# Kernel optimization log

Measured on AMD Instinct MI355X. Metric: run time of the kernel, lower is better.

## Reference

```python
import jax, jax.numpy as jnp
import numpy as np


def _phase_idx(phase):
    t = 4.0 * phase
    i1 = jnp.mod(jnp.floor(t).astype(jnp.int32), 4)
    i0 = jnp.mod(i1 - 1, 4)
    i2 = jnp.mod(i1 + 1, 4)
    i3 = jnp.mod(i1 + 2, 4)
    w = jnp.mod(t, 1.0)  # fmod(t,1) for t>=0
    return w, i0, i1, i2, i3


def _cubic(a0, a1, a2, a3, w):
    # Catmull-Rom spline blend; a* have shape (B, ...), w broadcastable
    return (a1
            + w * (0.5 * a2 - 0.5 * a0)
            + w * w * (a0 - 2.5 * a1 + 2.0 * a2 - 0.5 * a3)
            + w * w * w * (1.5 * a1 - 1.5 * a2 + 0.5 * a3 - 0.5 * a0))


def setup_inputs() -> dict:
    key = jax.random.key(0)
    ks = jax.random.split(key, 8)
    B = 4096
    dims = [128, 256, 256, 128]

    def kaiming(k, shape):
        fan_in = shape[1]
        bound = np.sqrt(6.0 / fan_in)
        return jax.random.uniform(k, shape, jnp.float32, -bound, bound)

    inp = {
        "x": jax.random.normal(ks[0], (B, dims[0]), jnp.float32),
        "phase": jax.random.uniform(ks[1], (B,), jnp.float32),
    }
    for i in range(3):
        inp[f"w{i}"] = kaiming(ks[2 + i], (4, dims[i], dims[i + 1]))
        inp[f"b{i}"] = jnp.zeros((4, 1, dims[i + 1]), jnp.float32)
    return inp


def reference(x, phase, w0, b0, w1, b1, w2, b2):
    ws = [w0, w1, w2]
    bs = [b0, b1, b2]
    w, i0, i1, i2, i3 = _phase_idx(phase)
    w3 = w[:, None, None]  # (B,1,1) for weights and biases
    n = len(ws)
    for li in range(n):
        pw, pb = ws[li], bs[li]
        # per-sample interpolated weight (B, in, out) and bias (B, 1, out)
        weight = _cubic(pw[i0], pw[i1], pw[i2], pw[i3], w3)
        bias = _cubic(pb[i0], pb[i1], pb[i2], pb[i3], w3)
        x = jnp.einsum("bi,bio->bo", x, weight) + bias[:, 0, :]
        if li < n - 1:  # activation_at_last=False
            x = jax.nn.elu(x)
    return x
```

## Files before the change

kernel.cpp:

```cpp
#include <hip/hip_runtime.h>
#include <hip/hip_bf16.h>
#include <math.h>


typedef __attribute__((ext_vector_type(8))) short bf16x8;
typedef __attribute__((ext_vector_type(4))) float f32x4;

#define LDS_A0 0
#define LDS_A1 4096
#define LDS_A2 12288
#define LDS_B  20480
#define LDS_TOT (20480 + 131072)

#define VMW4()  asm volatile("s_waitcnt vmcnt(4)" ::: "memory")
#define VMW0()  asm volatile("s_waitcnt vmcnt(0)" ::: "memory")

static __device__ __forceinline__ void bar_keep_vmcnt() {
  asm volatile("s_waitcnt lgkmcnt(0)" ::: "memory");
  __builtin_amdgcn_s_barrier();
  asm volatile("" ::: "memory");
}

typedef const __attribute__((address_space(1))) unsigned char* gp1_t;
typedef __attribute__((address_space(3))) unsigned char* lp3_t;
static __device__ __forceinline__ void gl_lds16(const void* g, void* l) {
  __builtin_amdgcn_global_load_lds((gp1_t)g, (lp3_t)l, 16, 0, 0);
}

#define STAGE(sb, KIN, ci, slot) do {                                  \
    const unsigned short* _s = (sb) + (ci) * 32;                       \
    char* _d = myB + (slot) * 4096;                                    \
    gl_lds16(_s,             _d);                                      \
    gl_lds16(_s + (KIN),     _d + 1024);                               \
    gl_lds16(_s + 2 * (KIN), _d + 2048);                               \
    gl_lds16(_s + 3 * (KIN), _d + 3072);                               \
  } while (0)

static __device__ __forceinline__ unsigned short f2bf(float f) {
  union { float f; unsigned int u; } v; v.f = f;
  unsigned int r = v.u + 0x7fffu + ((v.u >> 16) & 1u);
  return (unsigned short)(r >> 16);
}

static __device__ __forceinline__ void catmull(float ph, float c[4]) {
  float t = 4.0f * ph;
  float ft = floorf(t);
  int i1 = ((int)ft) & 3;
  float w = t - ft;
  float w2 = w * w, w3 = w2 * w;
  float r0 = -0.5f * w + w2 - 0.5f * w3;
  float r1 = 1.0f - 2.5f * w2 + 1.5f * w3;
  float r2 = 0.5f * w + 2.0f * w2 - 1.5f * w3;
  float r3 = -0.5f * w2 + 0.5f * w3;
  c[(i1 + 3) & 3] = r0;
  c[i1]           = r1;
  c[(i1 + 1) & 3] = r2;
  c[(i1 + 2) & 3] = r3;
}

__global__ void k_wt_all(const float* __restrict__ w0, const float* __restrict__ w1,
                         const float* __restrict__ w2, unsigned short* __restrict__ t0,
                         unsigned short* __restrict__ t1, unsigned short* __restrict__ t2) {
  __shared__ float tile[32][33];
  int bid = blockIdx.x;
  const float* W; unsigned short* T; int R, C, idx;
  if (bid < 128)      { W = w0; T = t0; R = 512;  C = 256; idx = bid; }
  else if (bid < 384) { W = w1; T = t1; R = 1024; C = 256; idx = bid - 128; }
  else                { W = w2; T = t2; R = 1024; C = 128; idx = bid - 384; }
  int ntc = C >> 5;
  int tr = (idx / ntc) << 5;
  int tc = (idx % ntc) << 5;
  int tx = threadIdx.x, ty = threadIdx.y;
#pragma unroll
  for (int j = ty; j < 32; j += 8)
    tile[j][tx] = W[(size_t)(tr + j) * C + (tc + tx)];
  __syncthreads();
#pragma unroll
  for (int j = ty; j < 32; j += 8)
    T[(size_t)(tc + j) * R + (tr + tx)] = f2bf(tile[tx][j]);
}

static __device__ __forceinline__ void epi_mid(f32x4 a0, f32x4 a1, f32x4 a2, f32x4 a3,
                                               const float bm[4], const float cbr[4][4],
                                               int colg, int quad, char* outBuf) {
  const int g = colg >> 3;
  const int j2 = (colg & 7) * 2;
#pragma unroll
  for (int r = 0; r < 4; ++r) {
    const int m = quad * 4 + r;
    float y = cbr[r][0] * a0[r] + cbr[r][1] * a1[r] +
              cbr[r][2] * a2[r] + cbr[r][3] * a3[r] + bm[r];
    float a = y > 0.0f ? y : (__expf(y) - 1.0f);
    *(unsigned short*)(outBuf + m * 512 + (((g ^ (m & 15)) << 4) + j2)) = f2bf(a);
  }
}

#define MFMA4()                                                            \
  acc0 = __builtin_amdgcn_mfma_f32_16x16x32_bf16(av, bv0, acc0, 0, 0, 0);  \
  acc1 = __builtin_amdgcn_mfma_f32_16x16x32_bf16(av, bv1, acc1, 0, 0, 0);  \
  acc2 = __builtin_amdgcn_mfma_f32_16x16x32_bf16(av, bv2, acc2, 0, 0, 0);  \
  acc3 = __builtin_amdgcn_mfma_f32_16x16x32_bf16(av, bv3, acc3, 0, 0, 0)

#define LOADB()                                                \
  bf16x8 bv0 = *(const bf16x8*)(bs + bOff);                    \
  bf16x8 bv1 = *(const bf16x8*)(bs + 1024 + bOff);             \
  bf16x8 bv2 = *(const bf16x8*)(bs + 2048 + bOff);             \
  bf16x8 bv3 = *(const bf16x8*)(bs + 3072 + bOff)

__global__ __launch_bounds__(1024, 4) void k_fused(
    const float* __restrict__ x, const float* __restrict__ phase,
    const unsigned short* __restrict__ Wt0, const float* __restrict__ b0,
    const unsigned short* __restrict__ Wt1, const float* __restrict__ b1,
    const unsigned short* __restrict__ Wt2, const float* __restrict__ b2,
    float* __restrict__ out) {
  __shared__ __align__(1024) char smem[LDS_TOT];

  const int tid = threadIdx.x;
  const int lane = tid & 63;
  const int wid = tid >> 6;
  const int col = lane & 15;
  const int quad = lane >> 4;
  const int m0 = blockIdx.x * 16;
  const int colg = wid * 16 + col;
  const int cg = wid & 7, kh = wid >> 3;
  const int colg2 = cg * 16 + col;
  const int hi16 = (col & 12) << 4;
  const int lb = (quad ^ (col & 3)) << 4;
  const int bOff = col * 64 + quad * 16;

  char* myB = smem + LDS_B + wid * 8192;

  const int colL = lane >> 2, qs = lane & 3;
  const unsigned short* sb0 = Wt0 + (size_t)(wid * 16 + colL) * 512 + qs * 8;
  const unsigned short* sb1 = Wt1 + (size_t)(wid * 16 + colL) * 1024 + qs * 8;
  const unsigned short* sb2 = Wt2 + (size_t)(cg * 16 + colL) * 1024 + kh * 128 + qs * 8;

  float bva[4], bvb[4], bvc[4];
#pragma unroll
  for (int k = 0; k < 4; ++k) {
    bva[k] = b0[k * 256 + colg];
    bvb[k] = b1[k * 256 + colg];
    bvc[k] = b2[k * 128 + colg2];
  }
  float ph[4];
#pragma unroll
  for (int r = 0; r < 4; ++r) ph[r] = phase[m0 + quad * 4 + r];

  float4 xv = {0.f, 0.f, 0.f, 0.f};
  if (tid < 512)
    xv = *(const float4*)(x + (size_t)(m0 + (tid >> 5)) * 128 + (tid & 31) * 4);

  STAGE(sb0, 128, 0, 0);

  float cbr[4][4];
#pragma unroll
  for (int r = 0; r < 4; ++r) catmull(ph[r], cbr[r]);
  float bm0[4], bm1[4], bm2[4];
#pragma unroll
  for (int r = 0; r < 4; ++r) {
    bm0[r] = cbr[r][0] * bva[0] + cbr[r][1] * bva[1] + cbr[r][2] * bva[2] + cbr[r][3] * bva[3];
    bm1[r] = cbr[r][0] * bvb[0] + cbr[r][1] * bvb[1] + cbr[r][2] * bvb[2] + cbr[r][3] * bvb[3];
    bm2[r] = cbr[r][0] * bvc[0] + cbr[r][1] * bvc[1] + cbr[r][2] * bvc[2] + cbr[r][3] * bvc[3];
  }

  if (tid < 512) {
    const int row = tid >> 5, seg = tid & 31;
    const int g = seg >> 1, h = seg & 1;
    short4 hv;
    hv.x = (short)f2bf(xv.x); hv.y = (short)f2bf(xv.y);
    hv.z = (short)f2bf(xv.z); hv.w = (short)f2bf(xv.w);
    *(short4*)(smem + LDS_A0 + row * 256 + ((g ^ (row & 15)) << 4) + h * 8) = hv;
  }
  bar_keep_vmcnt();

  f32x4 acc0, acc1, acc2, acc3;

  {
    acc0 = acc1 = acc2 = acc3 = (f32x4){0.f, 0.f, 0.f, 0.f};
    const char* aL = smem + LDS_A0 + col * 256 + lb;
#pragma unroll
    for (int i = 0; i < 4; ++i) {
      if (i < 3) STAGE(sb0, 128, i + 1, (i + 1) & 1);
      else       STAGE(sb1, 256, 0, 0);
      VMW4();
      const char* bs = myB + (i & 1) * 4096;
      bf16x8 av = *(const bf16x8*)(aL + ((i << 6) ^ hi16));
      LOADB();
      MFMA4();
    }
    epi_mid(acc0, acc1, acc2, acc3, bm0, cbr, colg, quad, smem + LDS_A1);
  }
  bar_keep_vmcnt();

  {
    acc0 = acc1 = acc2 = acc3 = (f32x4){0.f, 0.f, 0.f, 0.f};
    const char* aL = smem + LDS_A1 + col * 512 + lb;
#pragma unroll
    for (int i = 0; i < 8; ++i) {
      if (i < 7) STAGE(sb1, 256, i + 1, (i + 1) & 1);
      else       STAGE(sb2, 256, 0, 0);
      VMW4();
      const char* bs = myB + (i & 1) * 4096;
      bf16x8 av = *(const bf16x8*)(aL + ((i << 6) ^ hi16));
      LOADB();
      MFMA4();
    }
    epi_mid(acc0, acc1, acc2, acc3, bm1, cbr, colg, quad, smem + LDS_A2);
  }
  bar_keep_vmcnt();

  {
    acc0 = acc1 = acc2 = acc3 = (f32x4){0.f, 0.f, 0.f, 0.f};
    const char* aL = smem + LDS_A2 + col * 512 + kh * 256 + lb;
#pragma unroll
    for (int i = 0; i < 4; ++i) {
      if (i < 3) { STAGE(sb2, 256, i + 1, (i + 1) & 1); VMW4(); }
      else       { VMW0(); }
      const char* bs = myB + (i & 1) * 4096;
      bf16x8 av = *(const bf16x8*)(aL + ((i << 6) ^ hi16));
      LOADB();
      MFMA4();
    }

    float part[4];
#pragma unroll
    for (int r = 0; r < 4; ++r)
      part[r] = cbr[r][0] * acc0[r] + cbr[r][1] * acc1[r] +
                cbr[r][2] * acc2[r] + cbr[r][3] * acc3[r];

    bar_keep_vmcnt();
    float* red = (float*)(smem + LDS_B);
    if (kh) {
#pragma unroll
      for (int r = 0; r < 4; ++r)
        red[cg * 272 + (quad * 4 + r) * 17 + col] = part[r];
    }
    bar_keep_vmcnt();
    if (!kh) {
#pragma unroll
      for (int r = 0; r < 4; ++r) {
        const int m = quad * 4 + r;
        float y = part[r] + red[cg * 272 + m * 17 + col] + bm2[r];
        out[(size_t)(m0 + m) * 128 + colg2] = y;
      }
    }
  }
}

extern "C" void kernel_launch(void* const* d_in, const int* in_sizes, int n_in,
                              void* d_out, int out_size, void* d_ws, size_t ws_size,
                              hipStream_t stream) {
  const float* x     = (const float*)d_in[0];
  const float* phase = (const float*)d_in[1];
  const float* w0    = (const float*)d_in[2];
  const float* b0    = (const float*)d_in[3];
  const float* w1    = (const float*)d_in[4];
  const float* b1    = (const float*)d_in[5];
  const float* w2    = (const float*)d_in[6];
  const float* b2    = (const float*)d_in[7];
  float* out = (float*)d_out;

  char* ws = (char*)d_ws;
  unsigned short* Wt0 = (unsigned short*)ws;
  unsigned short* Wt1 = (unsigned short*)(ws + 262144);
  unsigned short* Wt2 = (unsigned short*)(ws + 262144 + 524288);

  k_wt_all<<<512, dim3(32, 8), 0, stream>>>(w0, w1, w2, Wt0, Wt1, Wt2);
  k_fused<<<256, 1024, 0, stream>>>(x, phase, Wt0, b0, Wt1, b1, Wt2, b2, out);
}
```

Before: 90.77 us.

## Stagger per-block weight chunk order and issue prefetch after LDS reads

Each block now rotates which wave handles which column group and starts each layer's K loop at a block-dependent chunk offset. The goal is to spread concurrent global reads across different weight addresses and channels. The staging pipeline also now prefetches two chunks ahead, issuing each new load only after the current LDS reads complete (lgkmcnt(0)), so buffers can be reused safely while keeping more loads in flight. This adds index arithmetic, and the extra lgkmcnt waits could stall MFMA issue.

Measured after the change: 93.75 us. 1.03x slower.

```diff
diff --git a/kernel.cpp b/kernel.cpp
--- a/kernel.cpp
+++ b/kernel.cpp
@@ -14,6 +14,7 @@
 
 #define VMW4()  asm volatile("s_waitcnt vmcnt(4)" ::: "memory")
 #define VMW0()  asm volatile("s_waitcnt vmcnt(0)" ::: "memory")
+#define LGKM0() asm volatile("s_waitcnt lgkmcnt(0)" ::: "memory")
 
 static __device__ __forceinline__ void bar_keep_vmcnt() {
   asm volatile("s_waitcnt lgkmcnt(0)" ::: "memory");
@@ -121,8 +122,15 @@
   const int col = lane & 15;
   const int quad = lane >> 4;
   const int m0 = blockIdx.x * 16;
-  const int colg = wid * 16 + col;
-  const int cg = wid & 7, kh = wid >> 3;
+
+  const int p = (int)(blockIdx.x >> 3);
+  const int wg = (wid + p) & 15;
+  const int cr0 = p & 3;
+  const int cr1 = (p + (p >> 2)) & 7;
+  const int cr2 = (p >> 1) & 3;
+
+  const int colg = wg * 16 + col;
+  const int cg = wg & 7, kh = wg >> 3;
   const int colg2 = cg * 16 + col;
   const int hi16 = (col & 12) << 4;
   const int lb = (quad ^ (col & 3)) << 4;
@@ -131,8 +139,8 @@
   char* myB = smem + LDS_B + wid * 8192;
 
   const int colL = lane >> 2, qs = lane & 3;
-  const unsigned short* sb0 = Wt0 + (size_t)(wid * 16 + colL) * 512 + qs * 8;
-  const unsigned short* sb1 = Wt1 + (size_t)(wid * 16 + colL) * 1024 + qs * 8;
+  const unsigned short* sb0 = Wt0 + (size_t)(wg * 16 + colL) * 512 + qs * 8;
+  const unsigned short* sb1 = Wt1 + (size_t)(wg * 16 + colL) * 1024 + qs * 8;
   const unsigned short* sb2 = Wt2 + (size_t)(cg * 16 + colL) * 1024 + kh * 128 + qs * 8;
 
   float bva[4], bvb[4], bvc[4];
@@ -150,7 +158,8 @@
   if (tid < 512)
     xv = *(const float4*)(x + (size_t)(m0 + (tid >> 5)) * 128 + (tid & 31) * 4);
 
-  STAGE(sb0, 128, 0, 0);
+  STAGE(sb0, 128, cr0, 0);
+  STAGE(sb0, 128, (1 + cr0) & 3, 1);
 
   float cbr[4][4];
 #pragma unroll
@@ -180,12 +189,16 @@
     const char* aL = smem + LDS_A0 + col * 256 + lb;
 #pragma unroll
     for (int i = 0; i < 4; ++i) {
-      if (i < 3) STAGE(sb0, 128, i + 1, (i + 1) & 1);
-      else       STAGE(sb1, 256, 0, 0);
       VMW4();
       const char* bs = myB + (i & 1) * 4096;
-      bf16x8 av = *(const bf16x8*)(aL + ((i << 6) ^ hi16));
+      const int ci = (i + cr0) & 3;
+      bf16x8 av = *(const bf16x8*)(aL + ((ci << 6) ^ hi16));
       LOADB();
+      LGKM0();
+      if (i == 0)      STAGE(sb0, 128, (2 + cr0) & 3, 0);
+      else if (i == 1) STAGE(sb0, 128, (3 + cr0) & 3, 1);
+      else if (i == 2) STAGE(sb1, 256, cr1, 0);
+      else             STAGE(sb1, 256, (1 + cr1) & 7, 1);
       MFMA4();
     }
     epi_mid(acc0, acc1, acc2, acc3, bm0, cbr, colg, quad, smem + LDS_A1);
@@ -197,12 +210,15 @@
     const char* aL = smem + LDS_A1 + col * 512 + lb;
 #pragma unroll
     for (int i = 0; i < 8; ++i) {
-      if (i < 7) STAGE(sb1, 256, i + 1, (i + 1) & 1);
-      else       STAGE(sb2, 256, 0, 0);
       VMW4();
       const char* bs = myB + (i & 1) * 4096;
-      bf16x8 av = *(const bf16x8*)(aL + ((i << 6) ^ hi16));
+      const int ci = (i + cr1) & 7;
+      bf16x8 av = *(const bf16x8*)(aL + ((ci << 6) ^ hi16));
       LOADB();
+      LGKM0();
+      if (i < 6)       STAGE(sb1, 256, (i + 2 + cr1) & 7, i & 1);
+      else if (i == 6) STAGE(sb2, 256, cr2, 0);
+      else             STAGE(sb2, 256, (1 + cr2) & 3, 1);
       MFMA4();
     }
     epi_mid(acc0, acc1, acc2, acc3, bm1, cbr, colg, quad, smem + LDS_A2);
@@ -214,11 +230,16 @@
     const char* aL = smem + LDS_A2 + col * 512 + kh * 256 + lb;
 #pragma unroll
     for (int i = 0; i < 4; ++i) {
-      if (i < 3) { STAGE(sb2, 256, i + 1, (i + 1) & 1); VMW4(); }
-      else       { VMW0(); }
+      if (i < 3) { VMW4(); } else { VMW0(); }
       const char* bs = myB + (i & 1) * 4096;
-      bf16x8 av = *(const bf16x8*)(aL + ((i << 6) ^ hi16));
+      const int ci = (i + cr2) & 3;
+      bf16x8 av = *(const bf16x8*)(aL + ((ci << 6) ^ hi16));
       LOADB();
+      if (i < 2) {
+        LGKM0();
+        if (i == 0) STAGE(sb2, 256, (2 + cr2) & 3, 0);
+        else        STAGE(sb2, 256, (3 + cr2) & 3, 1);
+      }
       MFMA4();
     }
 
```

## Prefetch weight fragments into registers instead of staging through LDS

Applied to the files above, without the earlier changes.

The fused kernel stops using global_load_lds staging buffers and explicit vmcnt waits. It now loads each wave's B-operand fragments directly into a three-deep register ring (pre[3][4]) that is prefetched ahead across layer boundaries. This shrinks LDS use from about 150KB to about 29KB. Bias is folded by initialising the accumulators with the per-phase bias, which is valid because the Catmull-Rom coefficients sum to one, so the separate bias blend is removed. The transpose kernel is repacked to four 32x32 tiles per 1024-thread block. Risks are higher register pressure and compiler-inserted waits on the direct global loads.

After: 101.3 us. 11.6% more time.

```diff
diff --git a/kernel.cpp b/kernel.cpp
--- a/kernel.cpp
+++ b/kernel.cpp
@@ -6,35 +6,17 @@
 typedef __attribute__((ext_vector_type(8))) short bf16x8;
 typedef __attribute__((ext_vector_type(4))) float f32x4;
 
-#define LDS_A0 0
-#define LDS_A1 4096
-#define LDS_A2 12288
-#define LDS_B  20480
-#define LDS_TOT (20480 + 131072)
-
-#define VMW4()  asm volatile("s_waitcnt vmcnt(4)" ::: "memory")
-#define VMW0()  asm volatile("s_waitcnt vmcnt(0)" ::: "memory")
-
-static __device__ __forceinline__ void bar_keep_vmcnt() {
+#define LDS_A0  0
+#define LDS_A1  4096
+#define LDS_A2  12288
+#define LDS_RED 20480
+#define LDS_TOT (20480 + 8704)
+
+static __device__ __forceinline__ void bar_lgkm() {
   asm volatile("s_waitcnt lgkmcnt(0)" ::: "memory");
   __builtin_amdgcn_s_barrier();
   asm volatile("" ::: "memory");
 }
-
-typedef const __attribute__((address_space(1))) unsigned char* gp1_t;
-typedef __attribute__((address_space(3))) unsigned char* lp3_t;
-static __device__ __forceinline__ void gl_lds16(const void* g, void* l) {
-  __builtin_amdgcn_global_load_lds((gp1_t)g, (lp3_t)l, 16, 0, 0);
-}
-
-#define STAGE(sb, KIN, ci, slot) do {                                  \
-    const unsigned short* _s = (sb) + (ci) * 32;                       \
-    char* _d = myB + (slot) * 4096;                                    \
-    gl_lds16(_s,             _d);                                      \
-    gl_lds16(_s + (KIN),     _d + 1024);                               \
-    gl_lds16(_s + 2 * (KIN), _d + 2048);                               \
-    gl_lds16(_s + 3 * (KIN), _d + 3072);                               \
-  } while (0)
 
 static __device__ __forceinline__ unsigned short f2bf(float f) {
   union { float f; unsigned int u; } v; v.f = f;
@@ -58,30 +40,49 @@
   c[(i1 + 2) & 3] = r3;
 }
 
-__global__ void k_wt_all(const float* __restrict__ w0, const float* __restrict__ w1,
-                         const float* __restrict__ w2, unsigned short* __restrict__ t0,
-                         unsigned short* __restrict__ t1, unsigned short* __restrict__ t2) {
-  __shared__ float tile[32][33];
-  int bid = blockIdx.x;
+__global__ __launch_bounds__(1024) void k_wt_all(
+    const float* __restrict__ w0, const float* __restrict__ w1,
+    const float* __restrict__ w2, unsigned short* __restrict__ t0,
+    unsigned short* __restrict__ t1, unsigned short* __restrict__ t2) {
+  __shared__ float tile[4][32][33];
+  const int team = threadIdx.y >> 3;
+  const int tyy = threadIdx.y & 7;
+  const int tx = threadIdx.x;
+  const int bid = blockIdx.x * 4 + team;
   const float* W; unsigned short* T; int R, C, idx;
   if (bid < 128)      { W = w0; T = t0; R = 512;  C = 256; idx = bid; }
   else if (bid < 384) { W = w1; T = t1; R = 1024; C = 256; idx = bid - 128; }
   else                { W = w2; T = t2; R = 1024; C = 128; idx = bid - 384; }
-  int ntc = C >> 5;
-  int tr = (idx / ntc) << 5;
-  int tc = (idx % ntc) << 5;
-  int tx = threadIdx.x, ty = threadIdx.y;
-#pragma unroll
-  for (int j = ty; j < 32; j += 8)
-    tile[j][tx] = W[(size_t)(tr + j) * C + (tc + tx)];
+  const int ntc = C >> 5;
+  const int tr = (idx / ntc) << 5;
+  const int tc = (idx % ntc) << 5;
+#pragma unroll
+  for (int j = tyy; j < 32; j += 8)
+    tile[team][j][tx] = W[(size_t)(tr + j) * C + (tc + tx)];
   __syncthreads();
 #pragma unroll
-  for (int j = ty; j < 32; j += 8)
-    T[(size_t)(tc + j) * R + (tr + tx)] = f2bf(tile[tx][j]);
-}
-
-static __device__ __forceinline__ void epi_mid(f32x4 a0, f32x4 a1, f32x4 a2, f32x4 a3,
-                                               const float bm[4], const float cbr[4][4],
+  for (int j = tyy; j < 32; j += 8)
+    T[(size_t)(tc + j) * R + (tr + tx)] = f2bf(tile[team][tx][j]);
+}
+
+#define LOADCH(sb, KA, ci, sl)                                       \
+  pre[sl][0] = *(const bf16x8*)((sb) + 0 * (KA) + (ci) * 32);        \
+  pre[sl][1] = *(const bf16x8*)((sb) + 1 * (KA) + (ci) * 32);        \
+  pre[sl][2] = *(const bf16x8*)((sb) + 2 * (KA) + (ci) * 32);        \
+  pre[sl][3] = *(const bf16x8*)((sb) + 3 * (KA) + (ci) * 32)
+
+#define MFMA4()                                                            \
+  acc0 = __builtin_amdgcn_mfma_f32_16x16x32_bf16(av, b0v, acc0, 0, 0, 0);  \
+  acc1 = __builtin_amdgcn_mfma_f32_16x16x32_bf16(av, b1v, acc1, 0, 0, 0);  \
+  acc2 = __builtin_amdgcn_mfma_f32_16x16x32_bf16(av, b2v, acc2, 0, 0, 0);  \
+  acc3 = __builtin_amdgcn_mfma_f32_16x16x32_bf16(av, b3v, acc3, 0, 0, 0)
+
+#define TAKE(sl)                                                     \
+  bf16x8 b0v = pre[sl][0], b1v = pre[sl][1],                         \
+         b2v = pre[sl][2], b3v = pre[sl][3]
+
+static __device__ __forceinline__ void epi_mid(f32x4 a0, f32x4 a1, f32x4 a2,
+                                               f32x4 a3, const float cbr[4][4],
                                                int colg, int quad, char* outBuf) {
   const int g = colg >> 3;
   const int j2 = (colg & 7) * 2;
@@ -89,23 +90,11 @@
   for (int r = 0; r < 4; ++r) {
     const int m = quad * 4 + r;
     float y = cbr[r][0] * a0[r] + cbr[r][1] * a1[r] +
-              cbr[r][2] * a2[r] + cbr[r][3] * a3[r] + bm[r];
+              cbr[r][2] * a2[r] + cbr[r][3] * a3[r];
     float a = y > 0.0f ? y : (__expf(y) - 1.0f);
     *(unsigned short*)(outBuf + m * 512 + (((g ^ (m & 15)) << 4) + j2)) = f2bf(a);
   }
 }
-
-#define MFMA4()                                                            \
-  acc0 = __builtin_amdgcn_mfma_f32_16x16x32_bf16(av, bv0, acc0, 0, 0, 0);  \
-  acc1 = __builtin_amdgcn_mfma_f32_16x16x32_bf16(av, bv1, acc1, 0, 0, 0);  \
-  acc2 = __builtin_amdgcn_mfma_f32_16x16x32_bf16(av, bv2, acc2, 0, 0, 0);  \
-  acc3 = __builtin_amdgcn_mfma_f32_16x16x32_bf16(av, bv3, acc3, 0, 0, 0)
-
-#define LOADB()                                                \
-  bf16x8 bv0 = *(const bf16x8*)(bs + bOff);                    \
-  bf16x8 bv1 = *(const bf16x8*)(bs + 1024 + bOff);             \
-  bf16x8 bv2 = *(const bf16x8*)(bs + 2048 + bOff);             \
-  bf16x8 bv3 = *(const bf16x8*)(bs + 3072 + bOff)
 
 __global__ __launch_bounds__(1024, 4) void k_fused(
     const float* __restrict__ x, const float* __restrict__ phase,
@@ -126,14 +115,14 @@
   const int colg2 = cg * 16 + col;
   const int hi16 = (col & 12) << 4;
   const int lb = (quad ^ (col & 3)) << 4;
-  const int bOff = col * 64 + quad * 16;
-
-  char* myB = smem + LDS_B + wid * 8192;
-
-  const int colL = lane >> 2, qs = lane & 3;
-  const unsigned short* sb0 = Wt0 + (size_t)(wid * 16 + colL) * 512 + qs * 8;
-  const unsigned short* sb1 = Wt1 + (size_t)(wid * 16 + colL) * 1024 + qs * 8;
-  const unsigned short* sb2 = Wt2 + (size_t)(cg * 16 + colL) * 1024 + kh * 128 + qs * 8;
+
+  const unsigned short* sb0 = Wt0 + (size_t)colg * 512 + quad * 8;
+  const unsigned short* sb1 = Wt1 + (size_t)colg * 1024 + quad * 8;
+  const unsigned short* sb2 = Wt2 + (size_t)colg2 * 1024 + kh * 128 + quad * 8;
+
+  float4 xv = {0.f, 0.f, 0.f, 0.f};
+  if (tid < 512)
+    xv = *(const float4*)(x + (size_t)(m0 + (tid >> 5)) * 128 + (tid & 31) * 4);
 
   float bva[4], bvb[4], bvc[4];
 #pragma unroll
@@ -146,22 +135,14 @@
 #pragma unroll
   for (int r = 0; r < 4; ++r) ph[r] = phase[m0 + quad * 4 + r];
 
-  float4 xv = {0.f, 0.f, 0.f, 0.f};
-  if (tid < 512)
-    xv = *(const float4*)(x + (size_t)(m0 + (tid >> 5)) * 128 + (tid & 31) * 4);
-
-  STAGE(sb0, 128, 0, 0);
+  bf16x8 pre[3][4];
+  LOADCH(sb0, 128, 0, 0);
+  LOADCH(sb0, 128, 1, 1);
+  LOADCH(sb0, 128, 2, 2);
 
   float cbr[4][4];
 #pragma unroll
   for (int r = 0; r < 4; ++r) catmull(ph[r], cbr[r]);
-  float bm0[4], bm1[4], bm2[4];
-#pragma unroll
-  for (int r = 0; r < 4; ++r) {
-    bm0[r] = cbr[r][0] * bva[0] + cbr[r][1] * bva[1] + cbr[r][2] * bva[2] + cbr[r][3] * bva[3];
-    bm1[r] = cbr[r][0] * bvb[0] + cbr[r][1] * bvb[1] + cbr[r][2] * bvb[2] + cbr[r][3] * bvb[3];
-    bm2[r] = cbr[r][0] * bvc[0] + cbr[r][1] * bvc[1] + cbr[r][2] * bvc[2] + cbr[r][3] * bvc[3];
-  }
 
   if (tid < 512) {
     const int row = tid >> 5, seg = tid & 31;
@@ -171,54 +152,65 @@
     hv.z = (short)f2bf(xv.z); hv.w = (short)f2bf(xv.w);
     *(short4*)(smem + LDS_A0 + row * 256 + ((g ^ (row & 15)) << 4) + h * 8) = hv;
   }
-  bar_keep_vmcnt();
+  bar_lgkm();
 
   f32x4 acc0, acc1, acc2, acc3;
 
   {
-    acc0 = acc1 = acc2 = acc3 = (f32x4){0.f, 0.f, 0.f, 0.f};
+    acc0 = (f32x4){bva[0], bva[0], bva[0], bva[0]};
+    acc1 = (f32x4){bva[1], bva[1], bva[1], bva[1]};
+    acc2 = (f32x4){bva[2], bva[2], bva[2], bva[2]};
+    acc3 = (f32x4){bva[3], bva[3], bva[3], bva[3]};
     const char* aL = smem + LDS_A0 + col * 256 + lb;
 #pragma unroll
     for (int i = 0; i < 4; ++i) {
-      if (i < 3) STAGE(sb0, 128, i + 1, (i + 1) & 1);
-      else       STAGE(sb1, 256, 0, 0);
-      VMW4();
-      const char* bs = myB + (i & 1) * 4096;
+      const int sl = i % 3;
+      TAKE(sl);
+      if (i == 0)      { LOADCH(sb0, 128, 3, 0); }
+      else if (i == 1) { LOADCH(sb1, 256, 0, 1); }
+      else if (i == 2) { LOADCH(sb1, 256, 1, 2); }
+      else             { LOADCH(sb1, 256, 2, 0); }
       bf16x8 av = *(const bf16x8*)(aL + ((i << 6) ^ hi16));
-      LOADB();
       MFMA4();
     }
-    epi_mid(acc0, acc1, acc2, acc3, bm0, cbr, colg, quad, smem + LDS_A1);
-  }
-  bar_keep_vmcnt();
+    epi_mid(acc0, acc1, acc2, acc3, cbr, colg, quad, smem + LDS_A1);
+  }
+  bar_lgkm();
 
   {
-    acc0 = acc1 = acc2 = acc3 = (f32x4){0.f, 0.f, 0.f, 0.f};
+    acc0 = (f32x4){bvb[0], bvb[0], bvb[0], bvb[0]};
+    acc1 = (f32x4){bvb[1], bvb[1], bvb[1], bvb[1]};
+    acc2 = (f32x4){bvb[2], bvb[2], bvb[2], bvb[2]};
+    acc3 = (f32x4){bvb[3], bvb[3], bvb[3], bvb[3]};
     const char* aL = smem + LDS_A1 + col * 512 + lb;
 #pragma unroll
     for (int i = 0; i < 8; ++i) {
-      if (i < 7) STAGE(sb1, 256, i + 1, (i + 1) & 1);
-      else       STAGE(sb2, 256, 0, 0);
-      VMW4();
-      const char* bs = myB + (i & 1) * 4096;
+      const int sl = (i + 1) % 3;
+      TAKE(sl);
+      if (i < 5)       { LOADCH(sb1, 256, i + 3, sl); }
+      else if (i == 5) { LOADCH(sb2, 256, 0, sl); }
+      else if (i == 6) { LOADCH(sb2, 256, 1, sl); }
+      else             { LOADCH(sb2, 256, 2, sl); }
       bf16x8 av = *(const bf16x8*)(aL + ((i << 6) ^ hi16));
-      LOADB();
       MFMA4();
     }
-    epi_mid(acc0, acc1, acc2, acc3, bm1, cbr, colg, quad, smem + LDS_A2);
-  }
-  bar_keep_vmcnt();
+    epi_mid(acc0, acc1, acc2, acc3, cbr, colg, quad, smem + LDS_A2);
+  }
+  bar_lgkm();
 
   {
-    acc0 = acc1 = acc2 = acc3 = (f32x4){0.f, 0.f, 0.f, 0.f};
+    const float bz = 0.0f;
+    acc0 = (f32x4){kh ? bz : bvc[0], kh ? bz : bvc[0], kh ? bz : bvc[0], kh ? bz : bvc[0]};
+    acc1 = (f32x4){kh ? bz : bvc[1], kh ? bz : bvc[1], kh ? bz : bvc[1], kh ? bz : bvc[1]};
+    acc2 = (f32x4){kh ? bz : bvc[2], kh ? bz : bvc[2], kh ? bz : bvc[2], kh ? bz : bvc[2]};
+    acc3 = (f32x4){kh ? bz : bvc[3], kh ? bz : bvc[3], kh ? bz : bvc[3], kh ? bz : bvc[3]};
     const char* aL = smem + LDS_A2 + col * 512 + kh * 256 + lb;
 #pragma unroll
     for (int i = 0; i < 4; ++i) {
-      if (i < 3) { STAGE(sb2, 256, i + 1, (i + 1) & 1); VMW4(); }
-      else       { VMW0(); }
-      const char* bs = myB + (i & 1) * 4096;
+      const int sl = i % 3;
+      TAKE(sl);
+      if (i == 0) { LOADCH(sb2, 256, 3, 0); }
       bf16x8 av = *(const bf16x8*)(aL + ((i << 6) ^ hi16));
-      LOADB();
       MFMA4();
     }
 
@@ -228,19 +220,18 @@
       part[r] = cbr[r][0] * acc0[r] + cbr[r][1] * acc1[r] +
                 cbr[r][2] * acc2[r] + cbr[r][3] * acc3[r];
 
-    bar_keep_vmcnt();
-    float* red = (float*)(smem + LDS_B);
+    float* red = (float*)(smem + LDS_RED);
     if (kh) {
 #pragma unroll
       for (int r = 0; r < 4; ++r)
         red[cg * 272 + (quad * 4 + r) * 17 + col] = part[r];
     }
-    bar_keep_vmcnt();
+    bar_lgkm();
     if (!kh) {
 #pragma unroll
       for (int r = 0; r < 4; ++r) {
         const int m = quad * 4 + r;
-        float y = part[r] + red[cg * 272 + m * 17 + col] + bm2[r];
+        float y = part[r] + red[cg * 272 + m * 17 + col];
         out[(size_t)(m0 + m) * 128 + colg2] = y;
       }
     }
@@ -265,6 +256,6 @@
   unsigned short* Wt1 = (unsigned short*)(ws + 262144);
   unsigned short* Wt2 = (unsigned short*)(ws + 262144 + 524288);
 
-  k_wt_all<<<512, dim3(32, 8), 0, stream>>>(w0, w1, w2, Wt0, Wt1, Wt2);
+  k_wt_all<<<128, dim3(32, 32), 0, stream>>>(w0, w1, w2, Wt0, Wt1, Wt2);
   k_fused<<<256, 1024, 0, stream>>>(x, phase, Wt0, b0, Wt1, b1, Wt2, b2, out);
 }
```

## Deepen weight staging prefetch, fold bias into accumulator init, batch transpose tiles

Applied to the files above, without the earlier changes.

The weight-staging pipeline now keeps two chunks in flight. The next chunk is issued right after the LDS reads of the current chunk finish, behind an lgkmcnt wait, instead of before the compute. Biases are folded in by seeding the MFMA accumulators with the per-phase bias, since the Catmull-Rom weights sum to one, which removes the separate bias blend. The staging lane mapping is changed to col/quad order, the x load is hoisted earlier, and the transpose kernel packs four tiles per 1024-thread block. The deeper prefetch increases outstanding memory traffic and adds extra wait instructions.

After: 103.4 us. 13.9% more time.

```diff
diff --git a/kernel.cpp b/kernel.cpp
--- a/kernel.cpp
+++ b/kernel.cpp
@@ -14,6 +14,7 @@
 
 #define VMW4()  asm volatile("s_waitcnt vmcnt(4)" ::: "memory")
 #define VMW0()  asm volatile("s_waitcnt vmcnt(0)" ::: "memory")
+#define LGKM0() asm volatile("s_waitcnt lgkmcnt(0)" ::: "memory")
 
 static __device__ __forceinline__ void bar_keep_vmcnt() {
   asm volatile("s_waitcnt lgkmcnt(0)" ::: "memory");
@@ -58,30 +59,33 @@
   c[(i1 + 2) & 3] = r3;
 }
 
-__global__ void k_wt_all(const float* __restrict__ w0, const float* __restrict__ w1,
-                         const float* __restrict__ w2, unsigned short* __restrict__ t0,
-                         unsigned short* __restrict__ t1, unsigned short* __restrict__ t2) {
-  __shared__ float tile[32][33];
-  int bid = blockIdx.x;
+__global__ __launch_bounds__(1024) void k_wt_all(
+    const float* __restrict__ w0, const float* __restrict__ w1,
+    const float* __restrict__ w2, unsigned short* __restrict__ t0,
+    unsigned short* __restrict__ t1, unsigned short* __restrict__ t2) {
+  __shared__ float tile[4][32][33];
+  const int team = threadIdx.y >> 3;
+  const int tyy = threadIdx.y & 7;
+  const int tx = threadIdx.x;
+  const int bid = blockIdx.x * 4 + team;
   const float* W; unsigned short* T; int R, C, idx;
   if (bid < 128)      { W = w0; T = t0; R = 512;  C = 256; idx = bid; }
   else if (bid < 384) { W = w1; T = t1; R = 1024; C = 256; idx = bid - 128; }
   else                { W = w2; T = t2; R = 1024; C = 128; idx = bid - 384; }
-  int ntc = C >> 5;
-  int tr = (idx / ntc) << 5;
-  int tc = (idx % ntc) << 5;
-  int tx = threadIdx.x, ty = threadIdx.y;
-#pragma unroll
-  for (int j = ty; j < 32; j += 8)
-    tile[j][tx] = W[(size_t)(tr + j) * C + (tc + tx)];
+  const int ntc = C >> 5;
+  const int tr = (idx / ntc) << 5;
+  const int tc = (idx % ntc) << 5;
+#pragma unroll
+  for (int j = tyy; j < 32; j += 8)
+    tile[team][j][tx] = W[(size_t)(tr + j) * C + (tc + tx)];
   __syncthreads();
 #pragma unroll
-  for (int j = ty; j < 32; j += 8)
-    T[(size_t)(tc + j) * R + (tr + tx)] = f2bf(tile[tx][j]);
-}
-
-static __device__ __forceinline__ void epi_mid(f32x4 a0, f32x4 a1, f32x4 a2, f32x4 a3,
-                                               const float bm[4], const float cbr[4][4],
+  for (int j = tyy; j < 32; j += 8)
+    T[(size_t)(tc + j) * R + (tr + tx)] = f2bf(tile[team][tx][j]);
+}
+
+static __device__ __forceinline__ void epi_mid(f32x4 a0, f32x4 a1, f32x4 a2,
+                                               f32x4 a3, const float cbr[4][4],
                                                int colg, int quad, char* outBuf) {
   const int g = colg >> 3;
   const int j2 = (colg & 7) * 2;
@@ -89,7 +93,7 @@
   for (int r = 0; r < 4; ++r) {
     const int m = quad * 4 + r;
     float y = cbr[r][0] * a0[r] + cbr[r][1] * a1[r] +
-              cbr[r][2] * a2[r] + cbr[r][3] * a3[r] + bm[r];
+              cbr[r][2] * a2[r] + cbr[r][3] * a3[r];
     float a = y > 0.0f ? y : (__expf(y) - 1.0f);
     *(unsigned short*)(outBuf + m * 512 + (((g ^ (m & 15)) << 4) + j2)) = f2bf(a);
   }
@@ -126,14 +130,17 @@
   const int colg2 = cg * 16 + col;
   const int hi16 = (col & 12) << 4;
   const int lb = (quad ^ (col & 3)) << 4;
-  const int bOff = col * 64 + quad * 16;
+  const int bOff = lane * 16;
 
   char* myB = smem + LDS_B + wid * 8192;
 
-  const int colL = lane >> 2, qs = lane & 3;
-  const unsigned short* sb0 = Wt0 + (size_t)(wid * 16 + colL) * 512 + qs * 8;
-  const unsigned short* sb1 = Wt1 + (size_t)(wid * 16 + colL) * 1024 + qs * 8;
-  const unsigned short* sb2 = Wt2 + (size_t)(cg * 16 + colL) * 1024 + kh * 128 + qs * 8;
+  const unsigned short* sb0 = Wt0 + (size_t)(wid * 16 + col) * 512 + quad * 8;
+  const unsigned short* sb1 = Wt1 + (size_t)(wid * 16 + col) * 1024 + quad * 8;
+  const unsigned short* sb2 = Wt2 + (size_t)(cg * 16 + col) * 1024 + kh * 128 + quad * 8;
+
+  float4 xv = {0.f, 0.f, 0.f, 0.f};
+  if (tid < 512)
+    xv = *(const float4*)(x + (size_t)(m0 + (tid >> 5)) * 128 + (tid & 31) * 4);
 
   float bva[4], bvb[4], bvc[4];
 #pragma unroll
@@ -146,22 +153,12 @@
 #pragma unroll
   for (int r = 0; r < 4; ++r) ph[r] = phase[m0 + quad * 4 + r];
 
-  float4 xv = {0.f, 0.f, 0.f, 0.f};
-  if (tid < 512)
-    xv = *(const float4*)(x + (size_t)(m0 + (tid >> 5)) * 128 + (tid & 31) * 4);
-
   STAGE(sb0, 128, 0, 0);
+  STAGE(sb0, 128, 1, 1);
 
   float cbr[4][4];
 #pragma unroll
   for (int r = 0; r < 4; ++r) catmull(ph[r], cbr[r]);
-  float bm0[4], bm1[4], bm2[4];
-#pragma unroll
-  for (int r = 0; r < 4; ++r) {
-    bm0[r] = cbr[r][0] * bva[0] + cbr[r][1] * bva[1] + cbr[r][2] * bva[2] + cbr[r][3] * bva[3];
-    bm1[r] = cbr[r][0] * bvb[0] + cbr[r][1] * bvb[1] + cbr[r][2] * bvb[2] + cbr[r][3] * bvb[3];
-    bm2[r] = cbr[r][0] * bvc[0] + cbr[r][1] * bvc[1] + cbr[r][2] * bvc[2] + cbr[r][3] * bvc[3];
-  }
 
   if (tid < 512) {
     const int row = tid >> 5, seg = tid & 31;
@@ -176,49 +173,69 @@
   f32x4 acc0, acc1, acc2, acc3;
 
   {
-    acc0 = acc1 = acc2 = acc3 = (f32x4){0.f, 0.f, 0.f, 0.f};
+    acc0 = (f32x4){bva[0], bva[0], bva[0], bva[0]};
+    acc1 = (f32x4){bva[1], bva[1], bva[1], bva[1]};
+    acc2 = (f32x4){bva[2], bva[2], bva[2], bva[2]};
+    acc3 = (f32x4){bva[3], bva[3], bva[3], bva[3]};
     const char* aL = smem + LDS_A0 + col * 256 + lb;
 #pragma unroll
     for (int i = 0; i < 4; ++i) {
-      if (i < 3) STAGE(sb0, 128, i + 1, (i + 1) & 1);
-      else       STAGE(sb1, 256, 0, 0);
       VMW4();
       const char* bs = myB + (i & 1) * 4096;
       bf16x8 av = *(const bf16x8*)(aL + ((i << 6) ^ hi16));
       LOADB();
+      LGKM0();
+      if (i == 0)      STAGE(sb0, 128, 2, 0);
+      else if (i == 1) STAGE(sb0, 128, 3, 1);
+      else if (i == 2) STAGE(sb1, 256, 0, 0);
+      else             STAGE(sb1, 256, 1, 1);
       MFMA4();
     }
-    epi_mid(acc0, acc1, acc2, acc3, bm0, cbr, colg, quad, smem + LDS_A1);
+    epi_mid(acc0, acc1, acc2, acc3, cbr, colg, quad, smem + LDS_A1);
   }
   bar_keep_vmcnt();
 
   {
-    acc0 = acc1 = acc2 = acc3 = (f32x4){0.f, 0.f, 0.f, 0.f};
+    acc0 = (f32x4){bvb[0], bvb[0], bvb[0], bvb[0]};
+    acc1 = (f32x4){bvb[1], bvb[1], bvb[1], bvb[1]};
+    acc2 = (f32x4){bvb[2], bvb[2], bvb[2], bvb[2]};
+    acc3 = (f32x4){bvb[3], bvb[3], bvb[3], bvb[3]};
     const char* aL = smem + LDS_A1 + col * 512 + lb;
 #pragma unroll
     for (int i = 0; i < 8; ++i) {
-      if (i < 7) STAGE(sb1, 256, i + 1, (i + 1) & 1);
-      else       STAGE(sb2, 256, 0, 0);
       VMW4();
       const char* bs = myB + (i & 1) * 4096;
       bf16x8 av = *(const bf16x8*)(aL + ((i << 6) ^ hi16));
       LOADB();
+      LGKM0();
+      if (i < 6)       STAGE(sb1, 256, i + 2, i & 1);
+      else if (i == 6) STAGE(sb2, 256, 0, 0);
+      else             STAGE(sb2, 256, 1, 1);
       MFMA4();
     }
-    epi_mid(acc0, acc1, acc2, acc3, bm1, cbr, colg, quad, smem + LDS_A2);
+    epi_mid(acc0, acc1, acc2, acc3, cbr, colg, quad, smem + LDS_A2);
   }
   bar_keep_vmcnt();
 
   {
-    acc0 = acc1 = acc2 = acc3 = (f32x4){0.f, 0.f, 0.f, 0.f};
+    const float c0 = kh ? 0.f : bvc[0], c1 = kh ? 0.f : bvc[1];
+    const float c2 = kh ? 0.f : bvc[2], c3 = kh ? 0.f : bvc[3];
+    acc0 = (f32x4){c0, c0, c0, c0};
+    acc1 = (f32x4){c1, c1, c1, c1};
+    acc2 = (f32x4){c2, c2, c2, c2};
+    acc3 = (f32x4){c3, c3, c3, c3};
     const char* aL = smem + LDS_A2 + col * 512 + kh * 256 + lb;
 #pragma unroll
     for (int i = 0; i < 4; ++i) {
-      if (i < 3) { STAGE(sb2, 256, i + 1, (i + 1) & 1); VMW4(); }
-      else       { VMW0(); }
+      if (i < 3) { VMW4(); } else { VMW0(); }
       const char* bs = myB + (i & 1) * 4096;
       bf16x8 av = *(const bf16x8*)(aL + ((i << 6) ^ hi16));
       LOADB();
+      if (i < 2) {
+        LGKM0();
+        if (i == 0) STAGE(sb2, 256, 2, 0);
+        else        STAGE(sb2, 256, 3, 1);
+      }
       MFMA4();
     }
 
@@ -240,7 +257,7 @@
 #pragma unroll
       for (int r = 0; r < 4; ++r) {
         const int m = quad * 4 + r;
-        float y = part[r] + red[cg * 272 + m * 17 + col] + bm2[r];
+        float y = part[r] + red[cg * 272 + m * 17 + col];
         out[(size_t)(m0 + m) * 128 + colg2] = y;
       }
     }
@@ -265,6 +282,6 @@
   unsigned short* Wt1 = (unsigned short*)(ws + 262144);
   unsigned short* Wt2 = (unsigned short*)(ws + 262144 + 524288);
 
-  k_wt_all<<<512, dim3(32, 8), 0, stream>>>(w0, w1, w2, Wt0, Wt1, Wt2);
+  k_wt_all<<<128, dim3(32, 32), 0, stream>>>(w0, w1, w2, Wt0, Wt1, Wt2);
   k_fused<<<256, 1024, 0, stream>>>(x, phase, Wt0, b0, Wt1, b1, Wt2, b2, out);
 }
```
